# Optimization experiments

Measured on AMD Instinct MI355X. Metric: run time of the kernel, lower is better.

Reference implementation:

```python
import jax, jax.numpy as jnp
import numpy as np

N_NODES = 100000
N_EDGES = 3200000
D_FEAT = 64
ALPHA = 0.1
K_STEPS = 10


def setup_inputs() -> dict:
    key = jax.random.key(0)
    k1, k2, k3, k4 = jax.random.split(key, 4)
    x = jax.random.normal(k1, (N_NODES, D_FEAT), dtype=jnp.float32)
    edge_row = jax.random.randint(k2, (N_EDGES,), 0, N_NODES, dtype=jnp.int32)
    edge_col = jax.random.randint(k3, (N_EDGES,), 0, N_NODES, dtype=jnp.int32)
    edge_weight = jax.random.uniform(k4, (N_EDGES,), dtype=jnp.float32)
    return {"x": x, "edge_row": edge_row, "edge_col": edge_col, "edge_weight": edge_weight}


def reference(x, edge_row, edge_col, edge_weight):
    # APPNP propagation: h <- (1-alpha) * A @ h + alpha * x, repeated K times.
    # A is sparse [N, N] given as an edge list; A @ h done via gather + segment_sum.
    def spmm(h):
        msgs = edge_weight[:, None] * h[edge_col]          # [E, d]
        return jax.ops.segment_sum(msgs, edge_row, num_segments=N_NODES)  # [N, d]

    h = x
    for _ in range(K_STEPS):
        h = (1.0 - ALPHA) * spmm(h) + ALPHA * x
    return h
```

## Files before the change

### kernel.cpp

```cpp
#include <hip/hip_runtime.h>

typedef unsigned int u32;
typedef unsigned long long u64;
typedef u32   v4u __attribute__((ext_vector_type(4)));
typedef float v4f __attribute__((ext_vector_type(4)));

#define NN 100000
#define NE 3200000
#define DF 64
#define ALPHA 0.1f
#define BETA 0.9f
#define K_STEPS 10
#define NBKT 782
#define EPT 16
#define CHUNK (256 * EPT)
#define NCHB ((NE + CHUNK - 1) / CHUNK)

__device__ __forceinline__ u32 rne_bf16(float f) {
    u32 u = __float_as_uint(f);
    return (u + 0x7FFFu + ((u >> 16) & 1u)) >> 16;
}
__device__ __forceinline__ float bf_lo(u32 w) { return __uint_as_float(w << 16); }
__device__ __forceinline__ float bf_hi(u32 w) { return __uint_as_float(w & 0xFFFF0000u); }

__global__ void bucket_hist(const int* __restrict__ row, int* __restrict__ bcnt) {
    __shared__ int s[NBKT];
    for (int i = threadIdx.x; i < NBKT; i += 256) s[i] = 0;
    __syncthreads();
    int base = blockIdx.x * CHUNK + threadIdx.x;
    #pragma unroll
    for (int j = 0; j < EPT; ++j) {
        int e = base + j * 256;
        if (e < NE) atomicAdd(&s[row[e] >> 7], 1);
    }
    __syncthreads();
    for (int i = threadIdx.x; i < NBKT; i += 256) {
        int v = s[i];
        if (v) atomicAdd(&bcnt[i], v);
    }
}

__global__ void scan_buckets(const int* __restrict__ bcnt, int* __restrict__ bbase,
                             int* __restrict__ bcur) {
    __shared__ int s[1024];
    int i = threadIdx.x;
    int v = (i < NBKT) ? bcnt[i] : 0;
    s[i] = v;
    __syncthreads();
    for (int off = 1; off < 1024; off <<= 1) {
        int t = (i >= off) ? s[i - off] : 0;
        __syncthreads();
        s[i] += t;
        __syncthreads();
    }
    if (i < NBKT) { int b = s[i] - v; bbase[i] = b; bcur[i] = b; }
}

__global__ void bucket_scatter(const int* __restrict__ row, const int* __restrict__ col,
                               const float* __restrict__ w, int* __restrict__ bcur,
                               u64* __restrict__ e64) {
    __shared__ int scnt[NBKT];
    __shared__ int sbase[NBKT];
    for (int i = threadIdx.x; i < NBKT; i += 256) scnt[i] = 0;
    __syncthreads();
    int base = blockIdx.x * CHUNK + threadIdx.x;
    int rows[EPT];
    #pragma unroll
    for (int j = 0; j < EPT; ++j) {
        int e = base + j * 256;
        int r = (e < NE) ? row[e] : -1;
        rows[j] = r;
        if (r >= 0) atomicAdd(&scnt[r >> 7], 1);
    }
    __syncthreads();
    for (int i = threadIdx.x; i < NBKT; i += 256) {
        int c = scnt[i];
        sbase[i] = c ? atomicAdd(&bcur[i], c) : 0;
    }
    __syncthreads();
    for (int i = threadIdx.x; i < NBKT; i += 256) scnt[i] = 0;
    __syncthreads();
    #pragma unroll
    for (int j = 0; j < EPT; ++j) {
        int e = base + j * 256;
        int r = rows[j];
        if (r >= 0) {
            int b = r >> 7;
            int rank = atomicAdd(&scnt[b], 1);
            u32 cw = ((u32)col[e] << 15) | (rne_bf16(w[e]) & 0x7FFFu);
            e64[sbase[b] + rank] = ((u64)(r & 127) << 32) | cw;
        }
    }
}

__global__ void build_rows(const u64* __restrict__ e64, const int* __restrict__ bcnt,
                           const int* __restrict__ bbase, u32* __restrict__ edgesF,
                           int* __restrict__ rp) {
    __shared__ int rc[128];
    __shared__ int rb[128];
    int b = blockIdx.x;
    int cnt = bcnt[b], base = bbase[b];
    if (threadIdx.x < 128) rc[threadIdx.x] = 0;
    __syncthreads();
    for (int e = threadIdx.x; e < cnt; e += 256)
        atomicAdd(&rc[(int)(e64[base + e] >> 32)], 1);
    __syncthreads();
    if (threadIdx.x < 128) rb[threadIdx.x] = rc[threadIdx.x];
    __syncthreads();
    for (int off = 1; off < 128; off <<= 1) {
        int t = (threadIdx.x < 128 && threadIdx.x >= off) ? rb[threadIdx.x - off] : 0;
        __syncthreads();
        if (threadIdx.x < 128) rb[threadIdx.x] += t;
        __syncthreads();
    }
    if (threadIdx.x < 128) {
        int r = b * 128 + threadIdx.x;
        if (r < NN) rp[r] = base + rb[threadIdx.x];
        rc[threadIdx.x] = rb[threadIdx.x] - rc[threadIdx.x];
    }
    __syncthreads();
    for (int e = threadIdx.x; e < cnt; e += 256) {
        u64 ent = e64[base + e];
        int pos = atomicAdd(&rc[(int)(ent >> 32)], 1);
        edgesF[base + pos] = (u32)ent;
    }
}

__global__ void conv_x(const float* __restrict__ x, u32* __restrict__ xb) {
    int t = blockIdx.x * blockDim.x + threadIdx.x;
    if (t >= NN * 8) return;
    const float4* src = (const float4*)(x + (size_t)t * 8);
    float4 a = src[0], b = src[1];
    uint4 o;
    o.x = rne_bf16(a.x) | (rne_bf16(a.y) << 16);
    o.y = rne_bf16(a.z) | (rne_bf16(a.w) << 16);
    o.z = rne_bf16(b.x) | (rne_bf16(b.y) << 16);
    o.w = rne_bf16(b.z) | (rne_bf16(b.w) << 16);
    *(uint4*)(xb + (size_t)t * 4) = o;
}

__global__ __launch_bounds__(256) void
gather_step(const int* __restrict__ rp, const u32* __restrict__ edges,
            const u32* __restrict__ h, const u32* __restrict__ xb,
            u32* __restrict__ hn, float* __restrict__ outf, int final_step) {
    int lane = threadIdx.x & 63;
    int node = blockIdx.x * 4 + (threadIdx.x >> 6);
    int slice = lane >> 3;
    int fg = lane & 7;

    int start = (node == 0) ? 0 : rp[node - 1];
    int end = rp[node];

    float a0=0.f,a1=0.f,a2=0.f,a3=0.f,a4=0.f,a5=0.f,a6=0.f,a7=0.f;
    #pragma unroll 2
    for (int e = start + slice; e < end; e += 8) {
        u32 ew = __builtin_nontemporal_load(edges + e);
        u32 c = ew >> 15;
        float wv = __uint_as_float((ew & 0x7FFFu) << 16);
        const uint4 hv = *(const uint4*)(h + ((size_t)c << 5) + (fg << 2));
        a0 += wv * bf_lo(hv.x); a1 += wv * bf_hi(hv.x);
        a2 += wv * bf_lo(hv.y); a3 += wv * bf_hi(hv.y);
        a4 += wv * bf_lo(hv.z); a5 += wv * bf_hi(hv.z);
        a6 += wv * bf_lo(hv.w); a7 += wv * bf_hi(hv.w);
    }
    for (int m = 8; m <= 32; m <<= 1) {
        a0 += __shfl_xor(a0, m, 64); a1 += __shfl_xor(a1, m, 64);
        a2 += __shfl_xor(a2, m, 64); a3 += __shfl_xor(a3, m, 64);
        a4 += __shfl_xor(a4, m, 64); a5 += __shfl_xor(a5, m, 64);
        a6 += __shfl_xor(a6, m, 64); a7 += __shfl_xor(a7, m, 64);
    }
    uint4 xv = *(const uint4*)(xb + ((size_t)node << 5) + (fg << 2));
    float o0 = BETA * a0 + ALPHA * bf_lo(xv.x);
    float o1 = BETA * a1 + ALPHA * bf_hi(xv.x);
    float o2 = BETA * a2 + ALPHA * bf_lo(xv.y);
    float o3 = BETA * a3 + ALPHA * bf_hi(xv.y);
    float o4 = BETA * a4 + ALPHA * bf_lo(xv.z);
    float o5 = BETA * a5 + ALPHA * bf_hi(xv.z);
    float o6 = BETA * a6 + ALPHA * bf_lo(xv.w);
    float o7 = BETA * a7 + ALPHA * bf_hi(xv.w);

    if (!final_step) {
        if (slice == 0) {
            v4u o;
            o.x = rne_bf16(o0) | (rne_bf16(o1) << 16);
            o.y = rne_bf16(o2) | (rne_bf16(o3) << 16);
            o.z = rne_bf16(o4) | (rne_bf16(o5) << 16);
            o.w = rne_bf16(o6) | (rne_bf16(o7) << 16);
            __builtin_nontemporal_store(o, (v4u*)(hn + ((size_t)node << 5) + (fg << 2)));
        }
    } else {
        if (slice < 2) {
            v4f v;
            if (slice) { v.x = o4; v.y = o5; v.z = o6; v.w = o7; }
            else       { v.x = o0; v.y = o1; v.z = o2; v.w = o3; }
            __builtin_nontemporal_store(v, (v4f*)(outf + (size_t)node * DF + fg * 8 + slice * 4));
        }
    }
}


extern "C" void kernel_launch(void* const* d_in, const int* in_sizes, int n_in,
                              void* d_out, int out_size, void* d_ws, size_t ws_size,
                              hipStream_t stream) {
    const float* x    = (const float*)d_in[0];
    const int*   erow = (const int*)  d_in[1];
    const int*   ecol = (const int*)  d_in[2];
    const float* ew   = (const float*)d_in[3];
    float* out = (float*)d_out;

    char* ws = (char*)d_ws;
    u32* edgesF = (u32*)(ws);
    u32* xb     = (u32*)(ws + 12800000);
    u32* hA     = (u32*)(ws + 25600000);
    u32* hB     = (u32*)(ws + 38400000);
    u64* e64    = (u64*)(ws + 25600000);
    int* rp     = (int*)(ws + 51200000);
    int* bcnt   = (int*)(ws + 51600000);
    int* bbase  = (int*)(ws + 51604096);
    int* bcur   = (int*)(ws + 51608192);

    dim3 blk(256);
    dim3 gChunk(NCHB);
    dim3 gConv((NN * 8 + 255) / 256);
    dim3 gG(NN / 4);

    (void)hipMemsetAsync(bcnt, 0, NBKT * sizeof(int), stream);
    bucket_hist<<<gChunk, blk, 0, stream>>>(erow, bcnt);
    scan_buckets<<<1, 1024, 0, stream>>>(bcnt, bbase, bcur);
    bucket_scatter<<<gChunk, blk, 0, stream>>>(erow, ecol, ew, bcur, e64);
    build_rows<<<NBKT, blk, 0, stream>>>(e64, bcnt, bbase, edgesF, rp);
    conv_x<<<gConv, blk, 0, stream>>>(x, xb);

    for (int k = 0; k < K_STEPS; ++k) {
        const u32* src = (k == 0) ? xb : ((k & 1) ? hA : hB);
        u32* dst = (k & 1) ? hB : hA;
        int fin = (k == K_STEPS - 1);
        gather_step<<<gG, blk, 0, stream>>>(rp, edgesF, src, xb,
                                            fin ? nullptr : dst,
                                            fin ? out : nullptr, fin);
    }
}
```

Baseline: 852.2 us.

## Partition edges by source-column segment for cache-local gathers with a reduce pass

```diff
diff --git a/kernel.cpp b/kernel.cpp
--- a/kernel.cpp
+++ b/kernel.cpp
@@ -11,7 +11,10 @@
 #define ALPHA 0.1f
 #define BETA 0.9f
 #define K_STEPS 10
-#define NBKT 782
+#define NSEG 4
+#define SEGW 25000
+#define NBKT_R 782
+#define NBKT_T (NSEG * NBKT_R)
 #define EPT 16
 #define CHUNK (256 * EPT)
 #define NCHB ((NE + CHUNK - 1) / CHUNK)
@@ -23,18 +26,22 @@
 __device__ __forceinline__ float bf_lo(u32 w) { return __uint_as_float(w << 16); }
 __device__ __forceinline__ float bf_hi(u32 w) { return __uint_as_float(w & 0xFFFF0000u); }
 
-__global__ void bucket_hist(const int* __restrict__ row, int* __restrict__ bcnt) {
-    __shared__ int s[NBKT];
-    for (int i = threadIdx.x; i < NBKT; i += 256) s[i] = 0;
+__global__ void bucket_hist(const int* __restrict__ row, const int* __restrict__ col,
+                            int* __restrict__ bcnt, int nseg) {
+    __shared__ int s[NBKT_T];
+    for (int i = threadIdx.x; i < NBKT_T; i += 256) s[i] = 0;
     __syncthreads();
     int base = blockIdx.x * CHUNK + threadIdx.x;
     #pragma unroll
     for (int j = 0; j < EPT; ++j) {
         int e = base + j * 256;
-        if (e < NE) atomicAdd(&s[row[e] >> 7], 1);
-    }
-    __syncthreads();
-    for (int i = threadIdx.x; i < NBKT; i += 256) {
+        if (e < NE) {
+            int seg = (nseg == 1) ? 0 : col[e] / SEGW;
+            atomicAdd(&s[seg * NBKT_R + (row[e] >> 7)], 1);
+        }
+    }
+    __syncthreads();
+    for (int i = threadIdx.x; i < NBKT_T; i += 256) {
         int v = s[i];
         if (v) atomicAdd(&bcnt[i], v);
     }
@@ -44,8 +51,14 @@
                              int* __restrict__ bcur) {
     __shared__ int s[1024];
     int i = threadIdx.x;
-    int v = (i < NBKT) ? bcnt[i] : 0;
-    s[i] = v;
+    int v[4]; int sum = 0;
+    #pragma unroll
+    for (int k = 0; k < 4; ++k) {
+        int idx = i * 4 + k;
+        v[k] = (idx < NBKT_T) ? bcnt[idx] : 0;
+        sum += v[k];
+    }
+    s[i] = sum;
     __syncthreads();
     for (int off = 1; off < 1024; off <<= 1) {
         int t = (i >= off) ? s[i - off] : 0;
@@ -53,52 +66,63 @@
         s[i] += t;
         __syncthreads();
     }
-    if (i < NBKT) { int b = s[i] - v; bbase[i] = b; bcur[i] = b; }
+    int run = s[i] - sum;
+    #pragma unroll
+    for (int k = 0; k < 4; ++k) {
+        int idx = i * 4 + k;
+        if (idx < NBKT_T) { bbase[idx] = run; bcur[idx] = run; }
+        run += v[k];
+    }
 }
 
 __global__ void bucket_scatter(const int* __restrict__ row, const int* __restrict__ col,
                                const float* __restrict__ w, int* __restrict__ bcur,
-                               u64* __restrict__ e64) {
-    __shared__ int scnt[NBKT];
-    __shared__ int sbase[NBKT];
-    for (int i = threadIdx.x; i < NBKT; i += 256) scnt[i] = 0;
+                               u64* __restrict__ e64, int nseg) {
+    __shared__ int scnt[NBKT_T];
+    __shared__ int sbase[NBKT_T];
+    for (int i = threadIdx.x; i < NBKT_T; i += 256) scnt[i] = 0;
     __syncthreads();
     int base = blockIdx.x * CHUNK + threadIdx.x;
-    int rows[EPT];
+    int bkt[EPT];
     #pragma unroll
     for (int j = 0; j < EPT; ++j) {
         int e = base + j * 256;
-        int r = (e < NE) ? row[e] : -1;
-        rows[j] = r;
-        if (r >= 0) atomicAdd(&scnt[r >> 7], 1);
-    }
-    __syncthreads();
-    for (int i = threadIdx.x; i < NBKT; i += 256) {
+        int b = -1;
+        if (e < NE) {
+            int seg = (nseg == 1) ? 0 : col[e] / SEGW;
+            b = seg * NBKT_R + (row[e] >> 7);
+            atomicAdd(&scnt[b], 1);
+        }
+        bkt[j] = b;
+    }
+    __syncthreads();
+    for (int i = threadIdx.x; i < NBKT_T; i += 256) {
         int c = scnt[i];
         sbase[i] = c ? atomicAdd(&bcur[i], c) : 0;
     }
     __syncthreads();
-    for (int i = threadIdx.x; i < NBKT; i += 256) scnt[i] = 0;
+    for (int i = threadIdx.x; i < NBKT_T; i += 256) scnt[i] = 0;
     __syncthreads();
     #pragma unroll
     for (int j = 0; j < EPT; ++j) {
         int e = base + j * 256;
-        int r = rows[j];
-        if (r >= 0) {
-            int b = r >> 7;
+        int b = bkt[j];
+        if (b >= 0) {
             int rank = atomicAdd(&scnt[b], 1);
             u32 cw = ((u32)col[e] << 15) | (rne_bf16(w[e]) & 0x7FFFu);
-            e64[sbase[b] + rank] = ((u64)(r & 127) << 32) | cw;
+            e64[sbase[b] + rank] = ((u64)(row[e] & 127) << 32) | cw;
         }
     }
 }
 
 __global__ void build_rows(const u64* __restrict__ e64, const int* __restrict__ bcnt,
                            const int* __restrict__ bbase, u32* __restrict__ edgesF,
-                           int* __restrict__ rp) {
+                           int* __restrict__ rp2) {
     __shared__ int rc[128];
     __shared__ int rb[128];
     int b = blockIdx.x;
+    int seg = b / NBKT_R;
+    int row0 = (b % NBKT_R) * 128;
     int cnt = bcnt[b], base = bbase[b];
     if (threadIdx.x < 128) rc[threadIdx.x] = 0;
     __syncthreads();
@@ -114,8 +138,8 @@
         __syncthreads();
     }
     if (threadIdx.x < 128) {
-        int r = b * 128 + threadIdx.x;
-        if (r < NN) rp[r] = base + rb[threadIdx.x];
+        int r = row0 + threadIdx.x;
+        if (r < NN) rp2[seg * NN + r] = base + rb[threadIdx.x];
         rc[threadIdx.x] = rb[threadIdx.x] - rc[threadIdx.x];
     }
     __syncthreads();
@@ -140,16 +164,19 @@
 }
 
 __global__ __launch_bounds__(256) void
-gather_step(const int* __restrict__ rp, const u32* __restrict__ edges,
-            const u32* __restrict__ h, const u32* __restrict__ xb,
-            u32* __restrict__ hn, float* __restrict__ outf, int final_step) {
+gather_seg(const int* __restrict__ rp2, const u32* __restrict__ edges,
+           const u32* __restrict__ h, u32* __restrict__ part) {
+    int m = blockIdx.x & 7;
+    int seg = m >> 1, half = m & 1;
+    int j = blockIdx.x >> 3;
+    int node = (j * 2 + half) * 4 + (threadIdx.x >> 6);
     int lane = threadIdx.x & 63;
-    int node = blockIdx.x * 4 + (threadIdx.x >> 6);
     int slice = lane >> 3;
     int fg = lane & 7;
 
-    int start = (node == 0) ? 0 : rp[node - 1];
-    int end = rp[node];
+    int g = seg * NN + node;
+    int start = (g == 0) ? 0 : rp2[g - 1];
+    int end = rp2[g];
 
     float a0=0.f,a1=0.f,a2=0.f,a3=0.f,a4=0.f,a5=0.f,a6=0.f,a7=0.f;
     #pragma unroll 2
@@ -163,11 +190,90 @@
         a4 += wv * bf_lo(hv.z); a5 += wv * bf_hi(hv.z);
         a6 += wv * bf_lo(hv.w); a7 += wv * bf_hi(hv.w);
     }
-    for (int m = 8; m <= 32; m <<= 1) {
-        a0 += __shfl_xor(a0, m, 64); a1 += __shfl_xor(a1, m, 64);
-        a2 += __shfl_xor(a2, m, 64); a3 += __shfl_xor(a3, m, 64);
-        a4 += __shfl_xor(a4, m, 64); a5 += __shfl_xor(a5, m, 64);
-        a6 += __shfl_xor(a6, m, 64); a7 += __shfl_xor(a7, m, 64);
+    for (int msk = 8; msk <= 32; msk <<= 1) {
+        a0 += __shfl_xor(a0, msk, 64); a1 += __shfl_xor(a1, msk, 64);
+        a2 += __shfl_xor(a2, msk, 64); a3 += __shfl_xor(a3, msk, 64);
+        a4 += __shfl_xor(a4, msk, 64); a5 += __shfl_xor(a5, msk, 64);
+        a6 += __shfl_xor(a6, msk, 64); a7 += __shfl_xor(a7, msk, 64);
+    }
+    if (slice == 0) {
+        v4u o;
+        o.x = rne_bf16(a0) | (rne_bf16(a1) << 16);
+        o.y = rne_bf16(a2) | (rne_bf16(a3) << 16);
+        o.z = rne_bf16(a4) | (rne_bf16(a5) << 16);
+        o.w = rne_bf16(a6) | (rne_bf16(a7) << 16);
+        __builtin_nontemporal_store(o, (v4u*)(part + ((size_t)g << 5) + (fg << 2)));
+    }
+}
+
+__global__ void reduce_seg(const u32* __restrict__ part, const u32* __restrict__ xb,
+                           u32* __restrict__ hn, float* __restrict__ outf,
+                           int final_step) {
+    int t = blockIdx.x * blockDim.x + threadIdx.x;
+    if (t >= NN * 8) return;
+    int node = t >> 3, fg = t & 7;
+    size_t off = ((size_t)node << 5) + (fg << 2);
+    float a0=0,a1=0,a2=0,a3=0,a4=0,a5=0,a6=0,a7=0;
+    #pragma unroll
+    for (int s = 0; s < NSEG; ++s) {
+        uint4 p = *(const uint4*)(part + ((size_t)(s * NN) << 5) + off);
+        a0 += bf_lo(p.x); a1 += bf_hi(p.x);
+        a2 += bf_lo(p.y); a3 += bf_hi(p.y);
+        a4 += bf_lo(p.z); a5 += bf_hi(p.z);
+        a6 += bf_lo(p.w); a7 += bf_hi(p.w);
+    }
+    uint4 xv = *(const uint4*)(xb + off);
+    float o0 = BETA * a0 + ALPHA * bf_lo(xv.x);
+    float o1 = BETA * a1 + ALPHA * bf_hi(xv.x);
+    float o2 = BETA * a2 + ALPHA * bf_lo(xv.y);
+    float o3 = BETA * a3 + ALPHA * bf_hi(xv.y);
+    float o4 = BETA * a4 + ALPHA * bf_lo(xv.z);
+    float o5 = BETA * a5 + ALPHA * bf_hi(xv.z);
+    float o6 = BETA * a6 + ALPHA * bf_lo(xv.w);
+    float o7 = BETA * a7 + ALPHA * bf_hi(xv.w);
+    if (!final_step) {
+        v4u o;
+        o.x = rne_bf16(o0) | (rne_bf16(o1) << 16);
+        o.y = rne_bf16(o2) | (rne_bf16(o3) << 16);
+        o.z = rne_bf16(o4) | (rne_bf16(o5) << 16);
+        o.w = rne_bf16(o6) | (rne_bf16(o7) << 16);
+        __builtin_nontemporal_store(o, (v4u*)(hn + off));
+    } else {
+        float* dst = outf + (size_t)node * DF + fg * 8;
+        v4f va; va.x=o0; va.y=o1; va.z=o2; va.w=o3;
+        v4f vb; vb.x=o4; vb.y=o5; vb.z=o6; vb.w=o7;
+        __builtin_nontemporal_store(va, (v4f*)dst);
+        __builtin_nontemporal_store(vb, (v4f*)(dst + 4));
+    }
+}
+
+__global__ __launch_bounds__(256) void
+gather_step(const int* __restrict__ rp, const u32* __restrict__ edges,
+            const u32* __restrict__ h, const u32* __restrict__ xb,
+            u32* __restrict__ hn, float* __restrict__ outf, int final_step) {
+    int lane = threadIdx.x & 63;
+    int node = blockIdx.x * 4 + (threadIdx.x >> 6);
+    int slice = lane >> 3;
+    int fg = lane & 7;
+    int start = (node == 0) ? 0 : rp[node - 1];
+    int end = rp[node];
+    float a0=0.f,a1=0.f,a2=0.f,a3=0.f,a4=0.f,a5=0.f,a6=0.f,a7=0.f;
+    #pragma unroll 2
+    for (int e = start + slice; e < end; e += 8) {
+        u32 ew = __builtin_nontemporal_load(edges + e);
+        u32 c = ew >> 15;
+        float wv = __uint_as_float((ew & 0x7FFFu) << 16);
+        const uint4 hv = *(const uint4*)(h + ((size_t)c << 5) + (fg << 2));
+        a0 += wv * bf_lo(hv.x); a1 += wv * bf_hi(hv.x);
+        a2 += wv * bf_lo(hv.y); a3 += wv * bf_hi(hv.y);
+        a4 += wv * bf_lo(hv.z); a5 += wv * bf_hi(hv.z);
+        a6 += wv * bf_lo(hv.w); a7 += wv * bf_hi(hv.w);
+    }
+    for (int msk = 8; msk <= 32; msk <<= 1) {
+        a0 += __shfl_xor(a0, msk, 64); a1 += __shfl_xor(a1, msk, 64);
+        a2 += __shfl_xor(a2, msk, 64); a3 += __shfl_xor(a3, msk, 64);
+        a4 += __shfl_xor(a4, msk, 64); a5 += __shfl_xor(a5, msk, 64);
+        a6 += __shfl_xor(a6, msk, 64); a7 += __shfl_xor(a7, msk, 64);
     }
     uint4 xv = *(const uint4*)(xb + ((size_t)node << 5) + (fg << 2));
     float o0 = BETA * a0 + ALPHA * bf_lo(xv.x);
@@ -178,7 +284,6 @@
     float o5 = BETA * a5 + ALPHA * bf_hi(xv.z);
     float o6 = BETA * a6 + ALPHA * bf_lo(xv.w);
     float o7 = BETA * a7 + ALPHA * bf_hi(xv.w);
-
     if (!final_step) {
         if (slice == 0) {
             v4u o;
@@ -209,34 +314,51 @@
     float* out = (float*)d_out;
 
     char* ws = (char*)d_ws;
+    const int segm = (ws_size >= 92000000) ? 1 : 0;
+    const int nseg = segm ? NSEG : 1;
+
     u32* edgesF = (u32*)(ws);
     u32* xb     = (u32*)(ws + 12800000);
     u32* hA     = (u32*)(ws + 25600000);
     u32* hB     = (u32*)(ws + 38400000);
+    u32* part   = (u32*)(ws + 38400000);
     u64* e64    = (u64*)(ws + 25600000);
-    int* rp     = (int*)(ws + 51200000);
-    int* bcnt   = (int*)(ws + 51600000);
-    int* bbase  = (int*)(ws + 51604096);
-    int* bcur   = (int*)(ws + 51608192);
+    int* rp2    = (int*)(ws + (segm ? 89600000 : 51200000));
+    char* cbase = ws + (segm ? 91200000 : 51600000);
+    int* bcnt   = (int*)(cbase);
+    int* bbase  = (int*)(cbase + 12544);
+    int* bcur   = (int*)(cbase + 25088);
 
     dim3 blk(256);
     dim3 gChunk(NCHB);
     dim3 gConv((NN * 8 + 255) / 256);
-    dim3 gG(NN / 4);
-
-    (void)hipMemsetAsync(bcnt, 0, NBKT * sizeof(int), stream);
-    bucket_hist<<<gChunk, blk, 0, stream>>>(erow, bcnt);
+
+    (void)hipMemsetAsync(bcnt, 0, NBKT_T * sizeof(int), stream);
+    bucket_hist<<<gChunk, blk, 0, stream>>>(erow, ecol, bcnt, nseg);
     scan_buckets<<<1, 1024, 0, stream>>>(bcnt, bbase, bcur);
-    bucket_scatter<<<gChunk, blk, 0, stream>>>(erow, ecol, ew, bcur, e64);
-    build_rows<<<NBKT, blk, 0, stream>>>(e64, bcnt, bbase, edgesF, rp);
+    bucket_scatter<<<gChunk, blk, 0, stream>>>(erow, ecol, ew, bcur, e64, nseg);
+    build_rows<<<nseg * NBKT_R, blk, 0, stream>>>(e64, bcnt, bbase, edgesF, rp2);
     conv_x<<<gConv, blk, 0, stream>>>(x, xb);
 
-    for (int k = 0; k < K_STEPS; ++k) {
-        const u32* src = (k == 0) ? xb : ((k & 1) ? hA : hB);
-        u32* dst = (k & 1) ? hB : hA;
-        int fin = (k == K_STEPS - 1);
-        gather_step<<<gG, blk, 0, stream>>>(rp, edgesF, src, xb,
-                                            fin ? nullptr : dst,
-                                            fin ? out : nullptr, fin);
-    }
-}
+    if (segm) {
+        dim3 gP1(12500 * 8);
+        for (int k = 0; k < K_STEPS; ++k) {
+            const u32* src = (k == 0) ? xb : hA;
+            int fin = (k == K_STEPS - 1);
+            gather_seg<<<gP1, blk, 0, stream>>>(rp2, edgesF, src, part);
+            reduce_seg<<<gConv, blk, 0, stream>>>(part, xb,
+                                                  fin ? nullptr : hA,
+                                                  fin ? out : nullptr, fin);
+        }
+    } else {
+        dim3 gG(NN / 4);
+        for (int k = 0; k < K_STEPS; ++k) {
+            const u32* src = (k == 0) ? xb : ((k & 1) ? hA : hB);
+            u32* dst = (k & 1) ? hB : hA;
+            int fin = (k == K_STEPS - 1);
+            gather_step<<<gG, blk, 0, stream>>>(rp2, edgesF, src, xb,
+                                                fin ? nullptr : dst,
+                                                fin ? out : nullptr, fin);
+        }
+    }
+}
```

After: 1.672 ms. 96.2% more time.
